# Kernel optimization log

Hardware: AMD Instinct MI355X
Metric: run time of the kernel (lower is better)

## Reference

```python
import jax, jax.numpy as jnp
import numpy as np

N = 100_000   # nodes
E = 1_600_000 # edges per etype (avg degree 16)
D = 64        # in_size == out_size
NUM_ETYPES = 3


def setup_inputs() -> dict:
    key = jax.random.key(0)
    ks = jax.random.split(key, 1 + 3 * NUM_ETYPES)
    inp = {"x": jax.random.normal(ks[0], (N, D), dtype=jnp.float32)}
    for i in range(NUM_ETYPES):
        inp[f"W{i}"] = jax.random.normal(ks[1 + 3 * i], (D, D), dtype=jnp.float32) / np.sqrt(D)
        inp[f"b{i}"] = jnp.zeros((D,), dtype=jnp.float32)
        inp[f"src{i}"] = jax.random.randint(ks[2 + 3 * i], (E,), 0, N, dtype=jnp.int64 if jax.config.jax_enable_x64 else jnp.int32)
        inp[f"dst{i}"] = jax.random.randint(ks[3 + 3 * i], (E,), 0, N, dtype=jnp.int64 if jax.config.jax_enable_x64 else jnp.int32)
    return inp


def _etype_mean(x, W, b, src, dst):
    # per-etype linear transform: Wh = x @ W + b   [N, D]
    Wh = x @ W + b
    # copy_u: gather source features onto edges      [E, D]
    m = Wh[src]
    # mean reduce onto destination nodes (zero for zero-in-degree nodes, as in DGL)
    s = jax.ops.segment_sum(m, dst, num_segments=N)                       # [N, D]
    deg = jax.ops.segment_sum(jnp.ones((src.shape[0],), x.dtype), dst, num_segments=N)  # [N]
    deg = deg[:, None]
    return jnp.where(deg > 0, s / jnp.maximum(deg, 1.0), 0.0)


def reference(x, W0, b0, W1, b1, W2, b2, src0, dst0, src1, dst1, src2, dst2):
    # multi_update_all with 'sum' cross-etype reducer
    h = _etype_mean(x, W0, b0, src0, dst0)
    h = h + _etype_mean(x, W1, b1, src1, dst1)
    h = h + _etype_mean(x, W2, b2, src2, dst2)
    return h
```

## Files before the change

### kernel.cpp

```cpp
#include <hip/hip_runtime.h>

#define N_NODES 100000
#define E_EDGES 1600000
#define D 64
#define NB 256
#define BW 391
#define EPB 2048
#define NBLK ((E_EDGES + EPB - 1) / EPB)
#define CAP 8192
#define CSR_STRIDE (E_EDGES + 64)

__global__ __launch_bounds__(256) void hist_kernel(
    const int* __restrict__ dst0, const int* __restrict__ dst1, const int* __restrict__ dst2,
    unsigned* __restrict__ bh) {
    __shared__ unsigned h[NB];
    int t = threadIdx.x, blk = blockIdx.x, e = blockIdx.y;
    const int* dst = (e == 0) ? dst0 : (e == 1) ? dst1 : dst2;
    h[t] = 0;
    __syncthreads();
    int base = blk * EPB;
    #pragma unroll
    for (int r = 0; r < EPB / 256; ++r) {
        int i = base + r * 256 + t;
        if (i < E_EDGES) atomicAdd(&h[(unsigned)dst[i] / BW], 1u);
    }
    __syncthreads();
    bh[((size_t)e * NBLK + blk) * NB + t] = h[t];
}

__global__ __launch_bounds__(256) void colscan_kernel(
    unsigned* __restrict__ bh, unsigned* __restrict__ total) {
    __shared__ unsigned sa[1024], sb[1024];
    int t = threadIdx.x, b = blockIdx.x, e = blockIdx.y;
    unsigned orig[4];
    #pragma unroll
    for (int k = 0; k < 4; ++k) {
        int i = t + k * 256;
        unsigned v = (i < NBLK) ? bh[((size_t)e * NBLK + i) * NB + b] : 0u;
        orig[k] = v;
        sa[i] = v;
    }
    __syncthreads();
    unsigned* s = sa; unsigned* d = sb;
    for (int st = 1; st < 1024; st <<= 1) {
        #pragma unroll
        for (int k = 0; k < 4; ++k) {
            int i = t + k * 256;
            d[i] = s[i] + ((i >= st) ? s[i - st] : 0u);
        }
        __syncthreads();
        unsigned* tmp = s; s = d; d = tmp;
    }
    #pragma unroll
    for (int k = 0; k < 4; ++k) {
        int i = t + k * 256;
        if (i < NBLK) bh[((size_t)e * NBLK + i) * NB + b] = s[i] - orig[k];
    }
    if (t == 0) total[e * NB + b] = s[1023];
}

__global__ __launch_bounds__(256) void basescan_kernel(
    const unsigned* __restrict__ total, unsigned* __restrict__ bases) {
    __shared__ unsigned sa[NB], sb[NB];
    int t = threadIdx.x;
    for (int e = 0; e < 3; ++e) {
        unsigned v = total[e * NB + t];
        sa[t] = v;
        __syncthreads();
        unsigned* s = sa; unsigned* d = sb;
        for (int st = 1; st < NB; st <<= 1) {
            d[t] = s[t] + ((t >= st) ? s[t - st] : 0u);
            __syncthreads();
            unsigned* tmp = s; s = d; d = tmp;
        }
        bases[e * NB + t] = s[t] - v;
        __syncthreads();
    }
}

__global__ __launch_bounds__(256) void bin_kernel(
    const int* __restrict__ s0, const int* __restrict__ s1, const int* __restrict__ s2,
    const int* __restrict__ d0, const int* __restrict__ d1, const int* __restrict__ d2,
    const unsigned* __restrict__ bh, const unsigned* __restrict__ bases,
    unsigned* __restrict__ binned) {
    __shared__ unsigned basel[NB];
    __shared__ unsigned lc[NB];
    int t = threadIdx.x, blk = blockIdx.x, e = blockIdx.y;
    const int* src_ = (e == 0) ? s0 : (e == 1) ? s1 : s2;
    const int* dst_ = (e == 0) ? d0 : (e == 1) ? d1 : d2;
    basel[t] = bases[e * NB + t] + bh[((size_t)e * NBLK + blk) * NB + t];
    lc[t] = 0;
    __syncthreads();
    int base = blk * EPB;
    #pragma unroll
    for (int r = 0; r < EPB / 256; ++r) {
        int i = base + r * 256 + t;
        if (i < E_EDGES) {
            unsigned dd = (unsigned)dst_[i];
            unsigned b = dd / BW;
            unsigned dloc = dd - b * BW;
            unsigned rank = atomicAdd(&lc[b], 1u);
            binned[(size_t)e * E_EDGES + basel[b] + rank] = (unsigned)src_[i] | (dloc << 17);
        }
    }
}

__global__ __launch_bounds__(256) void csr_kernel(
    const unsigned* __restrict__ binned, const unsigned* __restrict__ total,
    const unsigned* __restrict__ bases, int* __restrict__ csr,
    unsigned* __restrict__ off, unsigned* __restrict__ cnt) {
    __shared__ unsigned lh[512], sa[512], sb[512];
    __shared__ unsigned loff[BW + 1], lc[BW + 1];
    __shared__ int cl[CAP];
    int t = threadIdx.x, b = blockIdx.x, e = blockIdx.y;
    unsigned n = total[e * NB + b];
    unsigned g = bases[e * NB + b];
    lh[t] = 0; lh[t + 256] = 0;
    for (int j = t; j < BW + 1; j += 256) lc[j] = 0;
    __syncthreads();
    const unsigned* bp = binned + (size_t)e * E_EDGES + g;
    for (unsigned i = t; i < n; i += 256) atomicAdd(&lh[bp[i] >> 17], 1u);
    __syncthreads();
    sa[t] = lh[t]; sa[t + 256] = lh[t + 256];
    __syncthreads();
    unsigned* s = sa; unsigned* d = sb;
    for (int st = 1; st < 512; st <<= 1) {
        d[t] = s[t] + ((t >= st) ? s[t - st] : 0u);
        int i2 = t + 256;
        d[i2] = s[i2] + ((i2 >= st) ? s[i2 - st] : 0u);
        __syncthreads();
        unsigned* tmp = s; s = d; d = tmp;
    }
    if (t < BW + 1 - 256) loff[t + 256] = s[t + 256] - lh[t + 256];
    loff[t] = s[t] - lh[t];
    __syncthreads();
    int* csre = csr + (size_t)e * CSR_STRIDE;
    if (n <= CAP) {
        for (unsigned i = t; i < n; i += 256) {
            unsigned v = bp[i];
            unsigned dl = v >> 17;
            unsigned r = atomicAdd(&lc[dl], 1u);
            cl[loff[dl] + r] = (int)(v & 0x1FFFFu);
        }
        __syncthreads();
        for (unsigned i = t; i < n; i += 256) csre[g + i] = cl[i];
    } else {
        for (unsigned i = t; i < n; i += 256) {
            unsigned v = bp[i];
            unsigned dl = v >> 17;
            unsigned r = atomicAdd(&lc[dl], 1u);
            csre[g + loff[dl] + r] = (int)(v & 0x1FFFFu);
        }
    }
    int node0 = b * BW;
    for (int j = t; j < BW; j += 256) {
        int nd = node0 + j;
        if (nd < N_NODES) {
            off[e * N_NODES + nd] = g + loff[j];
            cnt[e * N_NODES + nd] = lh[j];
        }
    }
}

__global__ __launch_bounds__(256) void convert_kernel(const float* __restrict__ x,
                                                      unsigned* __restrict__ xh) {
    int i = blockIdx.x * 256 + threadIdx.x;
    float2 v = *reinterpret_cast<const float2*>(x + (size_t)i * 2);
    unsigned lo = __float_as_uint(v.x), hi = __float_as_uint(v.y);
    lo = (lo + 0x7FFFu + ((lo >> 16) & 1u)) >> 16;
    hi = (hi + 0x7FFFu + ((hi >> 16) & 1u)) & 0xFFFF0000u;
    xh[i] = lo | hi;
}

__global__ __launch_bounds__(256) void gather_fused_kernel(
    const unsigned* __restrict__ xh, const int* __restrict__ csr,
    const unsigned* __restrict__ off, const unsigned* __restrict__ cnt,
    const float* __restrict__ W0, const float* __restrict__ W1, const float* __restrict__ W2,
    const float* __restrict__ b0, const float* __restrict__ b1, const float* __restrict__ b2,
    float* __restrict__ out) {
    __shared__ float aggL[8][D];
    __shared__ int cntL[8];

    int tid = threadIdx.x;
    int hw = tid >> 5, l = tid & 31;
    int wv = tid >> 6, lane = tid & 63;
    int nodebase = blockIdx.x * 8;

    float acc0 = 0.f, acc1 = 0.f;

    for (int e = 0; e < 3; ++e) {
        const float* W = (e == 0) ? W0 : (e == 1) ? W1 : W2;
        const float* bias = (e == 0) ? b0 : (e == 1) ? b1 : b2;

        int node = nodebase + hw;
        unsigned c = cnt[e * N_NODES + node];
        const int* idx = csr + (size_t)e * CSR_STRIDE + off[e * N_NODES + node];

        float s0 = 0.f, s1 = 0.f, s2 = 0.f, s3 = 0.f;
        float s4 = 0.f, s5 = 0.f, s6 = 0.f, s7 = 0.f;
        float t0 = 0.f, t1 = 0.f, t2 = 0.f, t3 = 0.f;
        float t4 = 0.f, t5 = 0.f, t6 = 0.f, t7 = 0.f;
        unsigned j = 0;
        for (; j + 8 <= c; j += 8) {
            int i0 = idx[j + 0], i1 = idx[j + 1], i2 = idx[j + 2], i3 = idx[j + 3];
            int i4 = idx[j + 4], i5 = idx[j + 5], i6 = idx[j + 6], i7 = idx[j + 7];
            unsigned u0 = xh[(size_t)i0 * 32 + l];
            unsigned u1 = xh[(size_t)i1 * 32 + l];
            unsigned u2 = xh[(size_t)i2 * 32 + l];
            unsigned u3 = xh[(size_t)i3 * 32 + l];
            unsigned u4 = xh[(size_t)i4 * 32 + l];
            unsigned u5 = xh[(size_t)i5 * 32 + l];
            unsigned u6 = xh[(size_t)i6 * 32 + l];
            unsigned u7 = xh[(size_t)i7 * 32 + l];
            s0 += __uint_as_float(u0 << 16); t0 += __uint_as_float(u0 & 0xFFFF0000u);
            s1 += __uint_as_float(u1 << 16); t1 += __uint_as_float(u1 & 0xFFFF0000u);
            s2 += __uint_as_float(u2 << 16); t2 += __uint_as_float(u2 & 0xFFFF0000u);
            s3 += __uint_as_float(u3 << 16); t3 += __uint_as_float(u3 & 0xFFFF0000u);
            s4 += __uint_as_float(u4 << 16); t4 += __uint_as_float(u4 & 0xFFFF0000u);
            s5 += __uint_as_float(u5 << 16); t5 += __uint_as_float(u5 & 0xFFFF0000u);
            s6 += __uint_as_float(u6 << 16); t6 += __uint_as_float(u6 & 0xFFFF0000u);
            s7 += __uint_as_float(u7 << 16); t7 += __uint_as_float(u7 & 0xFFFF0000u);
        }
        for (; j < c; ++j) {
            int i0 = idx[j];
            unsigned u0 = xh[(size_t)i0 * 32 + l];
            s0 += __uint_as_float(u0 << 16);
            t0 += __uint_as_float(u0 & 0xFFFF0000u);
        }
        float sc = c ? 1.0f / (float)c : 0.0f;
        float m0 = (((s0 + s1) + (s2 + s3)) + ((s4 + s5) + (s6 + s7))) * sc;
        float m1 = (((t0 + t1) + (t2 + t3)) + ((t4 + t5) + (t6 + t7))) * sc;
        *reinterpret_cast<float2*>(&aggL[hw][2 * l]) = make_float2(m0, m1);
        if (l == 0) cntL[hw] = (int)c;
        __syncthreads();

        float a0 = 0.f, a1 = 0.f;
        #pragma unroll
        for (int k = 0; k < D; ++k) {
            float wk = W[k * D + lane];
            a0 = fmaf(aggL[2 * wv][k], wk, a0);
            a1 = fmaf(aggL[2 * wv + 1][k], wk, a1);
        }
        float bl = bias[lane];
        if (cntL[2 * wv] > 0)     acc0 += a0 + bl;
        if (cntL[2 * wv + 1] > 0) acc1 += a1 + bl;
        __syncthreads();
    }

    size_t o0 = (size_t)(nodebase + 2 * wv) * D + lane;
    out[o0] = acc0;
    out[o0 + D] = acc1;
}

extern "C" void kernel_launch(void* const* d_in, const int* in_sizes, int n_in,
                              void* d_out, int out_size, void* d_ws, size_t ws_size,
                              hipStream_t stream) {
    const float* x = (const float*)d_in[0];
    const float* W[3] = {(const float*)d_in[1], (const float*)d_in[5], (const float*)d_in[9]};
    const float* b[3] = {(const float*)d_in[2], (const float*)d_in[6], (const float*)d_in[10]};
    const int* src[3] = {(const int*)d_in[3], (const int*)d_in[7], (const int*)d_in[11]};
    const int* dst[3] = {(const int*)d_in[4], (const int*)d_in[8], (const int*)d_in[12]};
    float* out = (float*)d_out;

    char* ws = (char*)d_ws;
    size_t o = 0;
    unsigned* bh = (unsigned*)(ws + o);     o += (size_t)3 * NBLK * NB * 4;
    unsigned* total = (unsigned*)(ws + o);  o += (size_t)3 * NB * 4;
    unsigned* bases = (unsigned*)(ws + o);  o += (size_t)3 * NB * 4;
    unsigned* binned = (unsigned*)(ws + o); o += (size_t)3 * E_EDGES * 4;
    unsigned* xh = binned;
    int* csr = (int*)(ws + o);              o += (size_t)3 * CSR_STRIDE * 4;
    unsigned* off = (unsigned*)(ws + o);    o += (size_t)3 * N_NODES * 4;
    unsigned* cnt = (unsigned*)(ws + o);    o += (size_t)3 * N_NODES * 4;

    dim3 gE(NBLK, 3);
    hist_kernel<<<gE, 256, 0, stream>>>(dst[0], dst[1], dst[2], bh);
    dim3 gC(NB, 3);
    colscan_kernel<<<gC, 256, 0, stream>>>(bh, total);
    basescan_kernel<<<1, 256, 0, stream>>>(total, bases);
    bin_kernel<<<gE, 256, 0, stream>>>(src[0], src[1], src[2], dst[0], dst[1], dst[2],
                                       bh, bases, binned);
    dim3 gK(NB, 3);
    csr_kernel<<<gK, 256, 0, stream>>>(binned, total, bases, csr, off, cnt);
    convert_kernel<<<N_NODES * 32 / 256, 256, 0, stream>>>(x, xh);
    gather_fused_kernel<<<N_NODES / 8, 256, 0, stream>>>(xh, csr, off, cnt,
                                                         W[0], W[1], W[2], b[0], b[1], b[2], out);
}
```

Measured before the change: 294.7 us.

## Use buffer loads with pre-scaled CSR offsets and batch all etype gathers

CSR entries now store byte offsets (node index shifted left by 7), and the gather uses AMD raw buffer loads through one resource descriptor, dropping 64-bit address arithmetic. The scalar tail loop becomes a single masked 8-wide block; out-of-range indices read padding or return zero from the bounded buffer and are multiplied by zero. The three etype gathers now run before one barrier, with aggregates kept in larger shared memory, so the transform loop no longer needs per-etype synchronisation. The cost is more shared memory and reads of stale CSR entries past each node's edge list.

```diff
diff --git a/kernel.cpp b/kernel.cpp
--- a/kernel.cpp
+++ b/kernel.cpp
@@ -9,6 +9,15 @@
 #define NBLK ((E_EDGES + EPB - 1) / EPB)
 #define CAP 8192
 #define CSR_STRIDE (E_EDGES + 64)
+
+__device__ __forceinline__ __amdgpu_buffer_rsrc_t make_rsrc(const void* p, unsigned bytes) {
+    return __builtin_amdgcn_make_buffer_rsrc(const_cast<void*>(p), (short)0,
+                                             (int)bytes,
+                                             0x00020000);
+}
+__device__ __forceinline__ unsigned buf_ld(__amdgpu_buffer_rsrc_t r, int voff) {
+    return __builtin_amdgcn_raw_buffer_load_b32(r, voff, 0, 0);
+}
 
 __global__ __launch_bounds__(256) void hist_kernel(
     const int* __restrict__ dst0, const int* __restrict__ dst1, const int* __restrict__ dst2,
@@ -140,7 +149,7 @@
             unsigned v = bp[i];
             unsigned dl = v >> 17;
             unsigned r = atomicAdd(&lc[dl], 1u);
-            cl[loff[dl] + r] = (int)(v & 0x1FFFFu);
+            cl[loff[dl] + r] = (int)((v & 0x1FFFFu) << 7);
         }
         __syncthreads();
         for (unsigned i = t; i < n; i += 256) csre[g + i] = cl[i];
@@ -149,7 +158,7 @@
             unsigned v = bp[i];
             unsigned dl = v >> 17;
             unsigned r = atomicAdd(&lc[dl], 1u);
-            csre[g + loff[dl] + r] = (int)(v & 0x1FFFFu);
+            csre[g + loff[dl] + r] = (int)((v & 0x1FFFFu) << 7);
         }
     }
     int node0 = b * BW;
@@ -172,27 +181,32 @@
     xh[i] = lo | hi;
 }
 
+#define UNPACK_ADD(u, s, tt) \
+    s += __uint_as_float((u) << 16); tt += __uint_as_float((u) & 0xFFFF0000u);
+#define UNPACK_FMA(m, u, s, tt) \
+    s = fmaf(m, __uint_as_float((u) << 16), s); \
+    tt = fmaf(m, __uint_as_float((u) & 0xFFFF0000u), tt);
+
 __global__ __launch_bounds__(256) void gather_fused_kernel(
     const unsigned* __restrict__ xh, const int* __restrict__ csr,
     const unsigned* __restrict__ off, const unsigned* __restrict__ cnt,
     const float* __restrict__ W0, const float* __restrict__ W1, const float* __restrict__ W2,
     const float* __restrict__ b0, const float* __restrict__ b1, const float* __restrict__ b2,
     float* __restrict__ out) {
-    __shared__ float aggL[8][D];
-    __shared__ int cntL[8];
+    __shared__ float aggL[3][8][D];
+    __shared__ int cntL[3][8];
 
     int tid = threadIdx.x;
     int hw = tid >> 5, l = tid & 31;
     int wv = tid >> 6, lane = tid & 63;
     int nodebase = blockIdx.x * 8;
-
-    float acc0 = 0.f, acc1 = 0.f;
-
+    int node = nodebase + hw;
+    int l4 = l * 4;
+
+    __amdgpu_buffer_rsrc_t srd = make_rsrc(xh, N_NODES * D * 2);
+
+    #pragma unroll
     for (int e = 0; e < 3; ++e) {
-        const float* W = (e == 0) ? W0 : (e == 1) ? W1 : W2;
-        const float* bias = (e == 0) ? b0 : (e == 1) ? b1 : b2;
-
-        int node = nodebase + hw;
         unsigned c = cnt[e * N_NODES + node];
         const int* idx = csr + (size_t)e * CSR_STRIDE + off[e * N_NODES + node];
 
@@ -200,51 +214,74 @@
         float s4 = 0.f, s5 = 0.f, s6 = 0.f, s7 = 0.f;
         float t0 = 0.f, t1 = 0.f, t2 = 0.f, t3 = 0.f;
         float t4 = 0.f, t5 = 0.f, t6 = 0.f, t7 = 0.f;
-        unsigned j = 0;
-        for (; j + 8 <= c; j += 8) {
-            int i0 = idx[j + 0], i1 = idx[j + 1], i2 = idx[j + 2], i3 = idx[j + 3];
-            int i4 = idx[j + 4], i5 = idx[j + 5], i6 = idx[j + 6], i7 = idx[j + 7];
-            unsigned u0 = xh[(size_t)i0 * 32 + l];
-            unsigned u1 = xh[(size_t)i1 * 32 + l];
-            unsigned u2 = xh[(size_t)i2 * 32 + l];
-            unsigned u3 = xh[(size_t)i3 * 32 + l];
-            unsigned u4 = xh[(size_t)i4 * 32 + l];
-            unsigned u5 = xh[(size_t)i5 * 32 + l];
-            unsigned u6 = xh[(size_t)i6 * 32 + l];
-            unsigned u7 = xh[(size_t)i7 * 32 + l];
-            s0 += __uint_as_float(u0 << 16); t0 += __uint_as_float(u0 & 0xFFFF0000u);
-            s1 += __uint_as_float(u1 << 16); t1 += __uint_as_float(u1 & 0xFFFF0000u);
-            s2 += __uint_as_float(u2 << 16); t2 += __uint_as_float(u2 & 0xFFFF0000u);
-            s3 += __uint_as_float(u3 << 16); t3 += __uint_as_float(u3 & 0xFFFF0000u);
-            s4 += __uint_as_float(u4 << 16); t4 += __uint_as_float(u4 & 0xFFFF0000u);
-            s5 += __uint_as_float(u5 << 16); t5 += __uint_as_float(u5 & 0xFFFF0000u);
-            s6 += __uint_as_float(u6 << 16); t6 += __uint_as_float(u6 & 0xFFFF0000u);
-            s7 += __uint_as_float(u7 << 16); t7 += __uint_as_float(u7 & 0xFFFF0000u);
-        }
-        for (; j < c; ++j) {
-            int i0 = idx[j];
-            unsigned u0 = xh[(size_t)i0 * 32 + l];
-            s0 += __uint_as_float(u0 << 16);
-            t0 += __uint_as_float(u0 & 0xFFFF0000u);
+
+        unsigned fb = c >> 3;
+        for (unsigned blk = 0; blk < fb; ++blk) {
+            const int* ip = idx + blk * 8;
+            int i0 = ip[0], i1 = ip[1], i2 = ip[2], i3 = ip[3];
+            int i4 = ip[4], i5 = ip[5], i6 = ip[6], i7 = ip[7];
+            unsigned u0 = buf_ld(srd, i0 + l4);
+            unsigned u1 = buf_ld(srd, i1 + l4);
+            unsigned u2 = buf_ld(srd, i2 + l4);
+            unsigned u3 = buf_ld(srd, i3 + l4);
+            unsigned u4 = buf_ld(srd, i4 + l4);
+            unsigned u5 = buf_ld(srd, i5 + l4);
+            unsigned u6 = buf_ld(srd, i6 + l4);
+            unsigned u7 = buf_ld(srd, i7 + l4);
+            UNPACK_ADD(u0, s0, t0) UNPACK_ADD(u1, s1, t1)
+            UNPACK_ADD(u2, s2, t2) UNPACK_ADD(u3, s3, t3)
+            UNPACK_ADD(u4, s4, t4) UNPACK_ADD(u5, s5, t5)
+            UNPACK_ADD(u6, s6, t6) UNPACK_ADD(u7, s7, t7)
+        }
+        if (c & 7) {
+            unsigned j = fb * 8;
+            const int* ip = idx + j;
+            int i0 = ip[0], i1 = ip[1], i2 = ip[2], i3 = ip[3];
+            int i4 = ip[4], i5 = ip[5], i6 = ip[6], i7 = ip[7];
+            unsigned u0 = buf_ld(srd, i0 + l4);
+            unsigned u1 = buf_ld(srd, i1 + l4);
+            unsigned u2 = buf_ld(srd, i2 + l4);
+            unsigned u3 = buf_ld(srd, i3 + l4);
+            unsigned u4 = buf_ld(srd, i4 + l4);
+            unsigned u5 = buf_ld(srd, i5 + l4);
+            unsigned u6 = buf_ld(srd, i6 + l4);
+            unsigned u7 = buf_ld(srd, i7 + l4);
+            float m0 = (j + 0 < c) ? 1.f : 0.f;
+            float m1 = (j + 1 < c) ? 1.f : 0.f;
+            float m2 = (j + 2 < c) ? 1.f : 0.f;
+            float m3 = (j + 3 < c) ? 1.f : 0.f;
+            float m4 = (j + 4 < c) ? 1.f : 0.f;
+            float m5 = (j + 5 < c) ? 1.f : 0.f;
+            float m6 = (j + 6 < c) ? 1.f : 0.f;
+            float m7 = (j + 7 < c) ? 1.f : 0.f;
+            UNPACK_FMA(m0, u0, s0, t0) UNPACK_FMA(m1, u1, s1, t1)
+            UNPACK_FMA(m2, u2, s2, t2) UNPACK_FMA(m3, u3, s3, t3)
+            UNPACK_FMA(m4, u4, s4, t4) UNPACK_FMA(m5, u5, s5, t5)
+            UNPACK_FMA(m6, u6, s6, t6) UNPACK_FMA(m7, u7, s7, t7)
         }
         float sc = c ? 1.0f / (float)c : 0.0f;
         float m0 = (((s0 + s1) + (s2 + s3)) + ((s4 + s5) + (s6 + s7))) * sc;
         float m1 = (((t0 + t1) + (t2 + t3)) + ((t4 + t5) + (t6 + t7))) * sc;
-        *reinterpret_cast<float2*>(&aggL[hw][2 * l]) = make_float2(m0, m1);
-        if (l == 0) cntL[hw] = (int)c;
-        __syncthreads();
-
+        *reinterpret_cast<float2*>(&aggL[e][hw][2 * l]) = make_float2(m0, m1);
+        if (l == 0) cntL[e][hw] = (int)c;
+    }
+    __syncthreads();
+
+    float acc0 = 0.f, acc1 = 0.f;
+    #pragma unroll
+    for (int e = 0; e < 3; ++e) {
+        const float* W = (e == 0) ? W0 : (e == 1) ? W1 : W2;
+        const float* bias = (e == 0) ? b0 : (e == 1) ? b1 : b2;
         float a0 = 0.f, a1 = 0.f;
         #pragma unroll
         for (int k = 0; k < D; ++k) {
             float wk = W[k * D + lane];
-            a0 = fmaf(aggL[2 * wv][k], wk, a0);
-            a1 = fmaf(aggL[2 * wv + 1][k], wk, a1);
+            a0 = fmaf(aggL[e][2 * wv][k], wk, a0);
+            a1 = fmaf(aggL[e][2 * wv + 1][k], wk, a1);
         }
         float bl = bias[lane];
-        if (cntL[2 * wv] > 0)     acc0 += a0 + bl;
-        if (cntL[2 * wv + 1] > 0) acc1 += a1 + bl;
-        __syncthreads();
+        if (cntL[e][2 * wv] > 0)     acc0 += a0 + bl;
+        if (cntL[e][2 * wv + 1] > 0) acc1 += a1 + bl;
     }
 
     size_t o0 = (size_t)(nodebase + 2 * wv) * D + lane;
```

After: 277.1 us, median of 2. 6.0% less time.
